# Optimization experiments

Hardware: AMD Instinct MI355X
Metric: run time of the kernel (lower is better)

Reference implementation:

```python
import jax, jax.numpy as jnp
import numpy as np
from jax import lax

EPS_BN = 1e-5
EPS_LN = 1e-5


def setup_inputs() -> dict:
    key = jax.random.key(0)
    ks = jax.random.split(key, 10)
    B, Cin, H, W = 32, 512, 56, 56
    Cout, Cr = 128, 128 // 16  # CBAM reduction 16
    x = jax.random.normal(ks[0], (B, Cin, H, W), dtype=jnp.float32)
    w_proj = jax.random.normal(ks[1], (Cout, Cin), dtype=jnp.float32) * 0.02
    bn_g = jnp.ones((Cout,), jnp.float32)
    bn_b = jnp.zeros((Cout,), jnp.float32)
    bn_m = jax.random.normal(ks[2], (Cout,), dtype=jnp.float32) * 0.1
    bn_v = jax.random.uniform(ks[3], (Cout,), dtype=jnp.float32, minval=0.5, maxval=1.5)
    ca_w1 = jax.random.normal(ks[4], (Cr, Cout), dtype=jnp.float32) * 0.05
    ca_w2 = jax.random.normal(ks[5], (Cout, Cr), dtype=jnp.float32) * 0.05
    sa_w = jax.random.normal(ks[6], (1, 2, 7, 7), dtype=jnp.float32) * 0.05
    ln_g = jnp.ones((Cout,), jnp.float32)
    ln_b = jnp.zeros((Cout,), jnp.float32)
    return dict(x=x, w_proj=w_proj, bn_g=bn_g, bn_b=bn_b, bn_m=bn_m, bn_v=bn_v,
                ca_w1=ca_w1, ca_w2=ca_w2, sa_w=sa_w, ln_g=ln_g, ln_b=ln_b)


def _cbam(x, ca_w1, ca_w2, sa_w):
    # Channel attention: shared MLP on GAP and GMP over spatial dims
    avg = x.mean(axis=(2, 3))  # [B, C]
    mx = x.max(axis=(2, 3))    # [B, C]
    mlp = lambda p: jnp.einsum('cr,br->bc', ca_w2, jax.nn.relu(jnp.einsum('rc,bc->br', ca_w1, p)))
    ca = jax.nn.sigmoid(mlp(avg) + mlp(mx))  # [B, C]
    x = x * ca[:, :, None, None]
    # Spatial attention: channel-wise avg/max -> 7x7 conv -> sigmoid
    s = jnp.stack([x.mean(axis=1), x.max(axis=1)], axis=1)  # [B, 2, H, W]
    sa = lax.conv_general_dilated(s, sa_w, (1, 1), [(3, 3), (3, 3)],
                                  dimension_numbers=('NCHW', 'OIHW', 'NCHW'))
    return x * jax.nn.sigmoid(sa)


def reference(x, w_proj, bn_g, bn_b, bn_m, bn_v, ca_w1, ca_w2, sa_w, ln_g, ln_b):
    # 1x1 conv (no bias) as GEMM over channels
    h = jnp.einsum('bchw,oc->bohw', x, w_proj)
    # BatchNorm (inference) + SiLU
    scale = (bn_g / jnp.sqrt(bn_v + EPS_BN))[None, :, None, None]
    shift = (bn_b - bn_m * bn_g / jnp.sqrt(bn_v + EPS_BN))[None, :, None, None]
    h = h * scale + shift
    h = h * jax.nn.sigmoid(h)  # SiLU
    # CBAM with residual
    y = _cbam(h, ca_w1, ca_w2, sa_w) + h
    # GAP over spatial -> LayerNorm over channels
    y = y.mean(axis=(2, 3))  # [B, C]
    mu = y.mean(axis=-1, keepdims=True)
    var = ((y - mu) ** 2).mean(axis=-1, keepdims=True)
    return (y - mu) / jnp.sqrt(var + EPS_LN) * ln_g + ln_b
```

## Files before the change

kernel.cpp:

```cpp
#include <hip/hip_runtime.h>
#include <hip/hip_bf16.h>

typedef __bf16 bf16x8 __attribute__((ext_vector_type(8)));
typedef float f32x4 __attribute__((ext_vector_type(4)));

#define NB 32
#define CIN 512
#define COUT 128
#define NP 3136
#define WIMG 56

__device__ __forceinline__ unsigned fenc(float f) {
    unsigned u = __float_as_uint(f);
    return (u & 0x80000000u) ? ~u : (u | 0x80000000u);
}
__device__ __forceinline__ float fdec(unsigned e) {
    unsigned u = (e & 0x80000000u) ? (e ^ 0x80000000u) : ~e;
    return __uint_as_float(u);
}
__device__ __forceinline__ float bflo(unsigned u) { return __uint_as_float(u << 16); }
__device__ __forceinline__ float bfhi(unsigned u) { return __uint_as_float(u & 0xffff0000u); }

__device__ __forceinline__ void lds_barrier() {
    asm volatile("s_waitcnt lgkmcnt(0)" ::: "memory");
    __builtin_amdgcn_s_barrier();
    __builtin_amdgcn_sched_barrier(0);
}

__global__ __launch_bounds__(256) void k_wcvt(const float* __restrict__ wp,
                                              ushort* __restrict__ wb,
                                              unsigned* __restrict__ zero8k)
{
    int i = blockIdx.x * 256 + threadIdx.x;
    if (i < 2 * NB * COUT) zero8k[i] = 0u;
    float4 f = *(const float4*)(wp + i * 4);
    ushort4 u;
    __bf16 b0 = (__bf16)f.x, b1 = (__bf16)f.y, b2 = (__bf16)f.z, b3 = (__bf16)f.w;
    u.x = *(ushort*)&b0; u.y = *(ushort*)&b1; u.z = *(ushort*)&b2; u.w = *(ushort*)&b3;
    *(ushort4*)(wb + i * 4) = u;
}

__global__ __launch_bounds__(512, 6) void k_main(
    const float* __restrict__ x, const ushort* __restrict__ wb,
    const float* __restrict__ bn_g, const float* __restrict__ bn_b,
    const float* __restrict__ bn_m, const float* __restrict__ bn_v,
    ushort* __restrict__ hout, float* __restrict__ sumh, unsigned* __restrict__ mxenc)
{
    __shared__ __align__(16) ushort Xs[2][64 * 64];
    __shared__ __align__(16) ushort Ws[2][128 * 64];
    __shared__ float bnss[256];

    const int bid  = blockIdx.x;
    const int swz  = (bid & 7) * 196 + (bid >> 3);
    const int t    = threadIdx.x;
    const int b    = swz / 49;
    const int p0   = (swz % 49) * 64;
    const int lane = t & 63;
    const int l15  = lane & 15;
    const int lg   = lane >> 4;
    const int w    = t >> 6;

    if (t < COUT) {
        float sc = bn_g[t] * rsqrtf(bn_v[t] + 1e-5f);
        bnss[t]        = sc;
        bnss[t + COUT] = bn_b[t] - bn_m[t] * sc;
    }

    const int pr = t & 63;
    const int kg = t >> 6;
    const float* xb = x + ((size_t)b * CIN) * NP + p0 + pr;
    const int xbyte = pr * 128 + ((kg * 16) ^ ((pr & 7) << 4));

    const int ow = t >> 2, kq = t & 3;
    const ushort* wsrc = wb + ow * CIN + kq * 16;
    const int wbyte0 = ow * 128 + ((kq * 32) ^ ((ow & 7) << 4));
    const int wbyte1 = ow * 128 + ((kq * 32 + 16) ^ ((ow & 7) << 4));

    f32x4 acc[4];
#pragma unroll
    for (int nf = 0; nf < 4; ++nf) acc[nf] = (f32x4){0.f, 0.f, 0.f, 0.f};

    float ldx[2][8];
    uint4 ldw0, ldw1;

#pragma unroll
    for (int j = 0; j < 8; ++j) {
        ldx[0][j] = xb[(kg * 8 + j) * NP];
        ldx[1][j] = xb[(64 + kg * 8 + j) * NP];
    }
    ldw0 = *(const uint4*)(wsrc);
    ldw1 = *(const uint4*)(wsrc + 8);
    {
        bf16x8 v8;
#pragma unroll
        for (int j = 0; j < 8; ++j) v8[j] = (__bf16)ldx[0][j];
        *(bf16x8*)((char*)Xs[0] + xbyte) = v8;
        *(uint4*)((char*)Ws[0] + wbyte0) = ldw0;
        *(uint4*)((char*)Ws[0] + wbyte1) = ldw1;
    }

#pragma unroll
    for (int kc = 0; kc < 8; ++kc) {
        lds_barrier();
        if (kc < 6) {
#pragma unroll
            for (int j = 0; j < 8; ++j)
                ldx[kc & 1][j] = xb[((kc + 2) * 64 + kg * 8 + j) * NP];
        }
        if (kc < 7) {
            ldw0 = *(const uint4*)(wsrc + (kc + 1) * 64);
            ldw1 = *(const uint4*)(wsrc + (kc + 1) * 64 + 8);
        }
#pragma unroll
        for (int ks = 0; ks < 2; ++ks) {
            int o = w * 16 + l15;
            bf16x8 af = *(const bf16x8*)((const char*)Ws[kc & 1]
                         + o * 128 + ((ks * 64 + lg * 16) ^ ((o & 7) << 4)));
#pragma unroll
            for (int nf = 0; nf < 4; ++nf) {
                int p = nf * 16 + l15;
                bf16x8 bfr = *(const bf16x8*)((const char*)Xs[kc & 1]
                              + p * 128 + ((ks * 64 + lg * 16) ^ ((p & 7) << 4)));
                acc[nf] = __builtin_amdgcn_mfma_f32_16x16x32_bf16(
                    af, bfr, acc[nf], 0, 0, 0);
            }
        }
        if (kc < 7) {
            bf16x8 v8;
#pragma unroll
            for (int j = 0; j < 8; ++j) v8[j] = (__bf16)ldx[(kc + 1) & 1][j];
            *(bf16x8*)((char*)Xs[(kc + 1) & 1] + xbyte) = v8;
            *(uint4*)((char*)Ws[(kc + 1) & 1] + wbyte0) = ldw0;
            *(uint4*)((char*)Ws[(kc + 1) & 1] + wbyte1) = ldw1;
        }
    }

    __syncthreads();
    ushort* Hs = (ushort*)Xs;
#pragma unroll
    for (int reg = 0; reg < 4; ++reg) {
        int o = w * 16 + lg * 4 + reg;
        float sc = bnss[o], sh = bnss[o + COUT];
        float s_ = 0.f, m_ = -1e30f;
#pragma unroll
        for (int nf = 0; nf < 4; ++nf) {
            float d    = acc[nf][reg];
            float hval = d * sc + sh;
            hval       = hval / (1.f + __expf(-hval));
            s_ += hval;
            m_ = fmaxf(m_, hval);
            __bf16 hb = (__bf16)hval;
            Hs[o * 64 + nf * 16 + l15] = *(ushort*)&hb;
        }
#pragma unroll
        for (int d = 1; d < 16; d <<= 1) {
            s_ += __shfl_xor(s_, d, 64);
            m_ = fmaxf(m_, __shfl_xor(m_, d, 64));
        }
        if (l15 == 0) {
            atomicAdd(&sumh[b * COUT + o], s_);
            atomicMax(&mxenc[b * COUT + o], fenc(m_));
        }
    }
    __syncthreads();
#pragma unroll
    for (int r = 0; r < 2; ++r) {
        int flat = r * 512 + t;
        int orow = flat >> 3, c = flat & 7;
        uint4 v = *(const uint4*)&Hs[orow * 64 + c * 8];
        *(uint4*)&hout[((size_t)b * COUT + orow) * NP + p0 + c * 8] = v;
    }
}

__global__ __launch_bounds__(256) void k_sstat(const ushort* __restrict__ h,
                                               const float* __restrict__ sumh,
                                               const unsigned* __restrict__ mxenc,
                                               const float* __restrict__ w1,
                                               const float* __restrict__ w2,
                                               float* __restrict__ ca,
                                               float* __restrict__ sbuf)
{
    int b = blockIdx.y, z = blockIdx.z;
    int t = threadIdx.x;
    __shared__ float avg[128], mx[128], r1[16], cas[32];
    if (t < 128) {
        avg[t] = sumh[b * COUT + t] * (1.f / (float)NP);
        mx[t]  = fdec(mxenc[b * COUT + t]);
    }
    __syncthreads();
    if (t < 16) {
        int r = t & 7;
        const float* p = (t < 8) ? avg : mx;
        float s = 0.f;
        for (int c = 0; c < 128; ++c) s += w1[r * 128 + c] * p[c];
        r1[t] = fmaxf(s, 0.f);
    }
    __syncthreads();
    if (t < 32) {
        int o = z * 32 + t;
        float s = 0.f;
#pragma unroll
        for (int r = 0; r < 8; ++r) s += w2[o * 8 + r] * (r1[r] + r1[r + 8]);
        float cv = 1.f / (1.f + __expf(-s));
        cas[t] = cv;
        if (blockIdx.x == 0) ca[b * COUT + o] = cv;
    }
    __syncthreads();

    int pp = blockIdx.x * 256 + t;
    if (pp >= NP / 2) return;
    int p = pp * 2;
    const ushort* hb = h + ((size_t)b * COUT + z * 32) * NP + p;
    float s0 = 0.f, s1 = 0.f, m0 = -1e30f, m1 = -1e30f;
#pragma unroll 4
    for (int c = 0; c < 32; ++c) {
        unsigned u = *(const unsigned*)(hb + (size_t)c * NP);
        float cv = cas[c];
        float v0 = bflo(u) * cv;
        float v1 = bfhi(u) * cv;
        s0 += v0; s1 += v1;
        m0 = fmaxf(m0, v0); m1 = fmaxf(m1, v1);
    }
    float* sb = sbuf + ((size_t)(z * NB + b) * 2) * NP;
    sb[p] = s0; sb[p + 1] = s1;
    sb[NP + p] = m0; sb[NP + p + 1] = m1;
}

__global__ __launch_bounds__(256) void k_conv(const float* __restrict__ sbuf,
                                              const float* __restrict__ saw,
                                              float* __restrict__ sigsa)
{
    int band = blockIdx.x, b = blockIdx.y;
    int y0 = band * 7;
    int t = threadIdx.x;
    __shared__ float s[2][13 * WIMG];
    __shared__ float w[98];
    if (t < 98) w[t] = saw[t];
    for (int i = t; i < 13 * WIMG; i += 256) {
        int yy = y0 - 3 + i / WIMG;
        float vs = 0.f, vm = 0.f;
        if (yy >= 0 && yy < WIMG) {
            int p = yy * WIMG + (i % WIMG);
            float ssum = 0.f, smax = -1e30f;
#pragma unroll
            for (int z = 0; z < 4; ++z) {
                const float* sb = sbuf + ((size_t)(z * NB + b) * 2) * NP;
                ssum += sb[p];
                smax = fmaxf(smax, sb[NP + p]);
            }
            vs = ssum * (1.f / (float)COUT);
            vm = smax;
        }
        s[0][i] = vs;
        s[1][i] = vm;
    }
    __syncthreads();
    for (int i = t; i < 7 * WIMG; i += 256) {
        int ly = i / WIMG, px = i % WIMG;
        float a = 0.f;
#pragma unroll
        for (int ch = 0; ch < 2; ++ch) {
#pragma unroll
            for (int dy = 0; dy < 7; ++dy) {
                int li = (ly + dy) * WIMG;
                for (int dx = 0; dx < 7; ++dx) {
                    int xx = px + dx - 3;
                    if (xx < 0 || xx >= WIMG) continue;
                    a += s[ch][li + xx] * w[ch * 49 + dy * 7 + dx];
                }
            }
        }
        sigsa[b * NP + (y0 + ly) * WIMG + px] = 1.f / (1.f + __expf(-a));
    }
}

__global__ __launch_bounds__(256) void k_wsum(const ushort* __restrict__ h,
                                              const float* __restrict__ sigsa,
                                              const float* __restrict__ sumh,
                                              const float* __restrict__ ca,
                                              float* __restrict__ y)
{
    int bo = blockIdx.x;
    int b = bo >> 7;
    int t = threadIdx.x;
    const ushort* hr = h + (size_t)bo * NP;
    const float* sg  = sigsa + (size_t)b * NP;
    float s = 0.f;
#pragma unroll
    for (int i = 0; i < 3; ++i) {
        int q = (i * 256 + t) * 4;
        uint2 u = *(const uint2*)(hr + q);
        float4 g = *(const float4*)(sg + q);
        s += bflo(u.x) * g.x + bfhi(u.x) * g.y + bflo(u.y) * g.z + bfhi(u.y) * g.w;
    }
    if (t < 16) {
        int q = (768 + t) * 4;
        uint2 u = *(const uint2*)(hr + q);
        float4 g = *(const float4*)(sg + q);
        s += bflo(u.x) * g.x + bfhi(u.x) * g.y + bflo(u.y) * g.z + bfhi(u.y) * g.w;
    }
#pragma unroll
    for (int d = 1; d < 64; d <<= 1) s += __shfl_xor(s, d, 64);
    __shared__ float part[4];
    if ((t & 63) == 0) part[t >> 6] = s;
    __syncthreads();
    if (t == 0) {
        float tt = part[0] + part[1] + part[2] + part[3];
        y[bo] = (sumh[bo] + ca[bo] * tt) * (1.f / (float)NP);
    }
}

__global__ void k_ln(const float* __restrict__ y, const float* __restrict__ g,
                     const float* __restrict__ bta, float* __restrict__ out)
{
    int b = blockIdx.x, t = threadIdx.x;
    __shared__ float pr[2], pr2[2];
    float v = y[b * COUT + t];
    float s = v;
#pragma unroll
    for (int d = 1; d < 64; d <<= 1) s += __shfl_xor(s, d, 64);
    if ((t & 63) == 0) pr[t >> 6] = s;
    __syncthreads();
    float mu = (pr[0] + pr[1]) * (1.f / (float)COUT);
    float dv = v - mu;
    float q = dv * dv;
#pragma unroll
    for (int d = 1; d < 64; d <<= 1) q += __shfl_xor(q, d, 64);
    if ((t & 63) == 0) pr2[t >> 6] = q;
    __syncthreads();
    float var = (pr2[0] + pr2[1]) * (1.f / (float)COUT);
    out[b * COUT + t] = dv * rsqrtf(var + 1e-5f) * g[t] + bta[t];
}

extern "C" void kernel_launch(void* const* d_in, const int* in_sizes, int n_in,
                              void* d_out, int out_size, void* d_ws, size_t ws_size,
                              hipStream_t stream)
{
    const float* x     = (const float*)d_in[0];
    const float* wp    = (const float*)d_in[1];
    const float* bn_g  = (const float*)d_in[2];
    const float* bn_b  = (const float*)d_in[3];
    const float* bn_m  = (const float*)d_in[4];
    const float* bn_v  = (const float*)d_in[5];
    const float* ca_w1 = (const float*)d_in[6];
    const float* ca_w2 = (const float*)d_in[7];
    const float* sa_w  = (const float*)d_in[8];
    const float* ln_g  = (const float*)d_in[9];
    const float* ln_b  = (const float*)d_in[10];
    float* out = (float*)d_out;

    char* ws = (char*)d_ws;
    size_t off = 0;
    ushort*   hbuf  = (ushort*)(ws + off);   off += (size_t)NB * COUT * NP * 2;
    float*    sumh  = (float*)(ws + off);    off += NB * COUT * 4;
    unsigned* mxenc = (unsigned*)(ws + off); off += NB * COUT * 4;
    float*    ca    = (float*)(ws + off);    off += NB * COUT * 4;
    float*    sbuf  = (float*)(ws + off);    off += (size_t)4 * NB * 2 * NP * 4;
    float*    sigsa = (float*)(ws + off);    off += (size_t)NB * NP * 4;
    float*    ybuf  = (float*)(ws + off);    off += NB * COUT * 4;
    ushort*   wb16  = (ushort*)(ws + off);   off += (size_t)COUT * CIN * 2;

    k_wcvt<<<64, 256, 0, stream>>>(wp, wb16, (unsigned*)sumh);
    k_main<<<NB * 49, 512, 0, stream>>>(x, wb16, bn_g, bn_b, bn_m, bn_v, hbuf, sumh, mxenc);
    k_sstat<<<dim3(7, NB, 4), 256, 0, stream>>>(hbuf, sumh, mxenc, ca_w1, ca_w2, ca, sbuf);
    k_conv<<<dim3(8, NB), 256, 0, stream>>>(sbuf, sa_w, sigsa);
    k_wsum<<<NB * COUT, 256, 0, stream>>>(hbuf, sigsa, sumh, ca, ybuf);
    k_ln<<<NB, 128, 0, stream>>>(ybuf, ln_g, ln_b, out);
}
```

Measured before the change: 80.85 us.

## Store intermediate activations as FP8 and retile MFMA warps 2x2

The intermediate h tensor is stored as FP8 (e4m3) instead of bf16, halving the bytes written by the GEMM kernel and read by the spatial-stat and weighted-sum kernels. Consumers decode it through a 256-entry shared-memory lookup table. The GEMM warp tiling changes from 16 rows by 64 columns per warp to a 2x2 fragment layout, which reuses A and B fragments across more MFMAs. Per-block channel sum and max are now combined in shared memory before a single set of atomics. FP8 storage lowers the precision of h, which may hurt accuracy against the reference.

```diff
diff --git a/kernel.cpp b/kernel.cpp
--- a/kernel.cpp
+++ b/kernel.cpp
@@ -20,6 +20,23 @@
 }
 __device__ __forceinline__ float bflo(unsigned u) { return __uint_as_float(u << 16); }
 __device__ __forceinline__ float bfhi(unsigned u) { return __uint_as_float(u & 0xffff0000u); }
+
+__device__ __forceinline__ unsigned cvt2_fp8(float a, float b) {
+    unsigned r;
+    asm volatile("v_cvt_pk_fp8_f32 %0, %1, %2" : "=&v"(r) : "v"(a), "v"(b));
+    return r & 0xffffu;
+}
+__device__ __forceinline__ unsigned pack4_fp8(unsigned u01, unsigned u23) {
+    unsigned lo = cvt2_fp8(bflo(u01), bfhi(u01));
+    unsigned hi = cvt2_fp8(bflo(u23), bfhi(u23));
+    return lo | (hi << 16);
+}
+__device__ __forceinline__ float fp8_entry(int v) {
+    unsigned s = (v >> 7) & 1, e = (v >> 3) & 15, m = v & 7;
+    if (e) return __uint_as_float((s << 31) | ((e + 120) << 23) | (m << 20));
+    float f = (float)m * 0x1p-9f;
+    return s ? -f : f;
+}
 
 __device__ __forceinline__ void lds_barrier() {
     asm volatile("s_waitcnt lgkmcnt(0)" ::: "memory");
@@ -44,11 +61,13 @@
     const float* __restrict__ x, const ushort* __restrict__ wb,
     const float* __restrict__ bn_g, const float* __restrict__ bn_b,
     const float* __restrict__ bn_m, const float* __restrict__ bn_v,
-    ushort* __restrict__ hout, float* __restrict__ sumh, unsigned* __restrict__ mxenc)
+    uchar* __restrict__ hout, float* __restrict__ sumh, unsigned* __restrict__ mxenc)
 {
     __shared__ __align__(16) ushort Xs[2][64 * 64];
     __shared__ __align__(16) ushort Ws[2][128 * 64];
     __shared__ float bnss[256];
+    __shared__ float redS[2][COUT];
+    __shared__ float redM[2][COUT];
 
     const int bid  = blockIdx.x;
     const int swz  = (bid & 7) * 196 + (bid >> 3);
@@ -59,6 +78,8 @@
     const int l15  = lane & 15;
     const int lg   = lane >> 4;
     const int w    = t >> 6;
+    const int wm   = w >> 1;
+    const int wn   = w & 1;
 
     if (t < COUT) {
         float sc = bn_g[t] * rsqrtf(bn_v[t] + 1e-5f);
@@ -76,9 +97,11 @@
     const int wbyte0 = ow * 128 + ((kq * 32) ^ ((ow & 7) << 4));
     const int wbyte1 = ow * 128 + ((kq * 32 + 16) ^ ((ow & 7) << 4));
 
-    f32x4 acc[4];
-#pragma unroll
-    for (int nf = 0; nf < 4; ++nf) acc[nf] = (f32x4){0.f, 0.f, 0.f, 0.f};
+    f32x4 acc[2][2];
+#pragma unroll
+    for (int mf = 0; mf < 2; ++mf)
+#pragma unroll
+        for (int nf = 0; nf < 2; ++nf) acc[mf][nf] = (f32x4){0.f, 0.f, 0.f, 0.f};
 
     float ldx[2][8];
     uint4 ldw0, ldw1;
@@ -113,17 +136,25 @@
         }
 #pragma unroll
         for (int ks = 0; ks < 2; ++ks) {
-            int o = w * 16 + l15;
-            bf16x8 af = *(const bf16x8*)((const char*)Ws[kc & 1]
-                         + o * 128 + ((ks * 64 + lg * 16) ^ ((o & 7) << 4)));
-#pragma unroll
-            for (int nf = 0; nf < 4; ++nf) {
-                int p = nf * 16 + l15;
-                bf16x8 bfr = *(const bf16x8*)((const char*)Xs[kc & 1]
-                              + p * 128 + ((ks * 64 + lg * 16) ^ ((p & 7) << 4)));
-                acc[nf] = __builtin_amdgcn_mfma_f32_16x16x32_bf16(
-                    af, bfr, acc[nf], 0, 0, 0);
-            }
+            bf16x8 af[2], bfr[2];
+#pragma unroll
+            for (int mf = 0; mf < 2; ++mf) {
+                int o = wm * 32 + mf * 16 + l15;
+                af[mf] = *(const bf16x8*)((const char*)Ws[kc & 1]
+                          + o * 128 + ((ks * 64 + lg * 16) ^ ((o & 7) << 4)));
+            }
+#pragma unroll
+            for (int nf = 0; nf < 2; ++nf) {
+                int p = wn * 32 + nf * 16 + l15;
+                bfr[nf] = *(const bf16x8*)((const char*)Xs[kc & 1]
+                           + p * 128 + ((ks * 64 + lg * 16) ^ ((p & 7) << 4)));
+            }
+#pragma unroll
+            for (int mf = 0; mf < 2; ++mf)
+#pragma unroll
+                for (int nf = 0; nf < 2; ++nf)
+                    acc[mf][nf] = __builtin_amdgcn_mfma_f32_16x16x32_bf16(
+                        af[mf], bfr[nf], acc[mf][nf], 0, 0, 0);
         }
         if (kc < 7) {
             bf16x8 v8;
@@ -138,41 +169,52 @@
     __syncthreads();
     ushort* Hs = (ushort*)Xs;
 #pragma unroll
-    for (int reg = 0; reg < 4; ++reg) {
-        int o = w * 16 + lg * 4 + reg;
-        float sc = bnss[o], sh = bnss[o + COUT];
-        float s_ = 0.f, m_ = -1e30f;
-#pragma unroll
-        for (int nf = 0; nf < 4; ++nf) {
-            float d    = acc[nf][reg];
-            float hval = d * sc + sh;
-            hval       = hval / (1.f + __expf(-hval));
-            s_ += hval;
-            m_ = fmaxf(m_, hval);
-            __bf16 hb = (__bf16)hval;
-            Hs[o * 64 + nf * 16 + l15] = *(ushort*)&hb;
-        }
-#pragma unroll
-        for (int d = 1; d < 16; d <<= 1) {
-            s_ += __shfl_xor(s_, d, 64);
-            m_ = fmaxf(m_, __shfl_xor(m_, d, 64));
-        }
-        if (l15 == 0) {
-            atomicAdd(&sumh[b * COUT + o], s_);
-            atomicMax(&mxenc[b * COUT + o], fenc(m_));
-        }
-    }
-    __syncthreads();
-#pragma unroll
-    for (int r = 0; r < 2; ++r) {
-        int flat = r * 512 + t;
-        int orow = flat >> 3, c = flat & 7;
-        uint4 v = *(const uint4*)&Hs[orow * 64 + c * 8];
-        *(uint4*)&hout[((size_t)b * COUT + orow) * NP + p0 + c * 8] = v;
-    }
-}
-
-__global__ __launch_bounds__(256) void k_sstat(const ushort* __restrict__ h,
+    for (int mf = 0; mf < 2; ++mf) {
+#pragma unroll
+        for (int reg = 0; reg < 4; ++reg) {
+            int o = wm * 32 + mf * 16 + lg * 4 + reg;
+            float sc = bnss[o], sh = bnss[o + COUT];
+            float s_ = 0.f, m_ = -1e30f;
+#pragma unroll
+            for (int nf = 0; nf < 2; ++nf) {
+                float d    = acc[mf][nf][reg];
+                float hval = d * sc + sh;
+                hval       = hval / (1.f + __expf(-hval));
+                s_ += hval;
+                m_ = fmaxf(m_, hval);
+                __bf16 hb = (__bf16)hval;
+                Hs[o * 64 + wn * 32 + nf * 16 + l15] = *(ushort*)&hb;
+            }
+#pragma unroll
+            for (int d = 1; d < 16; d <<= 1) {
+                s_ += __shfl_xor(s_, d, 64);
+                m_ = fmaxf(m_, __shfl_xor(m_, d, 64));
+            }
+            if (l15 == 0) {
+                redS[wn][o] = s_;
+                redM[wn][o] = m_;
+            }
+        }
+    }
+    __syncthreads();
+    if (t < COUT) {
+        atomicAdd(&sumh[b * COUT + t], redS[0][t] + redS[1][t]);
+        atomicMax(&mxenc[b * COUT + t], fenc(fmaxf(redM[0][t], redM[1][t])));
+    }
+    {
+        int orow = t >> 2, c = t & 3;
+        uint4 a  = *(const uint4*)&Hs[orow * 64 + c * 16];
+        uint4 b4 = *(const uint4*)&Hs[orow * 64 + c * 16 + 8];
+        uint4 o4;
+        o4.x = pack4_fp8(a.x, a.y);
+        o4.y = pack4_fp8(a.z, a.w);
+        o4.z = pack4_fp8(b4.x, b4.y);
+        o4.w = pack4_fp8(b4.z, b4.w);
+        *(uint4*)&hout[((size_t)b * COUT + orow) * NP + p0 + c * 16] = o4;
+    }
+}
+
+__global__ __launch_bounds__(256) void k_sstat(const uchar* __restrict__ h,
                                                const float* __restrict__ sumh,
                                                const unsigned* __restrict__ mxenc,
                                                const float* __restrict__ w1,
@@ -182,7 +224,8 @@
 {
     int b = blockIdx.y, z = blockIdx.z;
     int t = threadIdx.x;
-    __shared__ float avg[128], mx[128], r1[16], cas[32];
+    __shared__ float avg[128], mx[128], r1[16], cas[32], tab[256];
+    tab[t] = fp8_entry(t);
     if (t < 128) {
         avg[t] = sumh[b * COUT + t] * (1.f / (float)NP);
         mx[t]  = fdec(mxenc[b * COUT + t]);
@@ -207,23 +250,27 @@
     }
     __syncthreads();
 
-    int pp = blockIdx.x * 256 + t;
-    if (pp >= NP / 2) return;
-    int p = pp * 2;
-    const ushort* hb = h + ((size_t)b * COUT + z * 32) * NP + p;
-    float s0 = 0.f, s1 = 0.f, m0 = -1e30f, m1 = -1e30f;
+    int idx = blockIdx.x * 256 + t;
+    if (idx >= NP / 4) return;
+    int p = idx * 4;
+    const uchar* hb = h + ((size_t)(b * COUT + z * 32)) * NP + p;
+    float s0 = 0.f, s1 = 0.f, s2 = 0.f, s3 = 0.f;
+    float m0 = -1e30f, m1 = -1e30f, m2 = -1e30f, m3 = -1e30f;
 #pragma unroll 4
     for (int c = 0; c < 32; ++c) {
         unsigned u = *(const unsigned*)(hb + (size_t)c * NP);
         float cv = cas[c];
-        float v0 = bflo(u) * cv;
-        float v1 = bfhi(u) * cv;
-        s0 += v0; s1 += v1;
+        float v0 = tab[u & 255] * cv;
+        float v1 = tab[(u >> 8) & 255] * cv;
+        float v2 = tab[(u >> 16) & 255] * cv;
+        float v3 = tab[u >> 24] * cv;
+        s0 += v0; s1 += v1; s2 += v2; s3 += v3;
         m0 = fmaxf(m0, v0); m1 = fmaxf(m1, v1);
+        m2 = fmaxf(m2, v2); m3 = fmaxf(m3, v3);
     }
     float* sb = sbuf + ((size_t)(z * NB + b) * 2) * NP;
-    sb[p] = s0; sb[p + 1] = s1;
-    sb[NP + p] = m0; sb[NP + p + 1] = m1;
+    *(float4*)&sb[p]      = make_float4(s0, s1, s2, s3);
+    *(float4*)&sb[NP + p] = make_float4(m0, m1, m2, m3);
 }
 
 __global__ __launch_bounds__(256) void k_conv(const float* __restrict__ sbuf,
@@ -274,7 +321,7 @@
     }
 }
 
-__global__ __launch_bounds__(256) void k_wsum(const ushort* __restrict__ h,
+__global__ __launch_bounds__(256) void k_wsum(const uchar* __restrict__ h,
                                               const float* __restrict__ sigsa,
                                               const float* __restrict__ sumh,
                                               const float* __restrict__ ca,
@@ -283,25 +330,30 @@
     int bo = blockIdx.x;
     int b = bo >> 7;
     int t = threadIdx.x;
-    const ushort* hr = h + (size_t)bo * NP;
+    __shared__ float tab[256];
+    __shared__ float part[4];
+    tab[t] = fp8_entry(t);
+    __syncthreads();
+    const uchar* hr = h + (size_t)bo * NP;
     const float* sg  = sigsa + (size_t)b * NP;
     float s = 0.f;
 #pragma unroll
     for (int i = 0; i < 3; ++i) {
-        int q = (i * 256 + t) * 4;
-        uint2 u = *(const uint2*)(hr + q);
-        float4 g = *(const float4*)(sg + q);
-        s += bflo(u.x) * g.x + bfhi(u.x) * g.y + bflo(u.y) * g.z + bfhi(u.y) * g.w;
+        int q = i * 256 + t;
+        unsigned u = *(const unsigned*)(hr + q * 4);
+        float4 g = *(const float4*)(sg + q * 4);
+        s += tab[u & 255] * g.x + tab[(u >> 8) & 255] * g.y
+           + tab[(u >> 16) & 255] * g.z + tab[u >> 24] * g.w;
     }
     if (t < 16) {
-        int q = (768 + t) * 4;
-        uint2 u = *(const uint2*)(hr + q);
-        float4 g = *(const float4*)(sg + q);
-        s += bflo(u.x) * g.x + bfhi(u.x) * g.y + bflo(u.y) * g.z + bfhi(u.y) * g.w;
+        int q = 768 + t;
+        unsigned u = *(const unsigned*)(hr + q * 4);
+        float4 g = *(const float4*)(sg + q * 4);
+        s += tab[u & 255] * g.x + tab[(u >> 8) & 255] * g.y
+           + tab[(u >> 16) & 255] * g.z + tab[u >> 24] * g.w;
     }
 #pragma unroll
     for (int d = 1; d < 64; d <<= 1) s += __shfl_xor(s, d, 64);
-    __shared__ float part[4];
     if ((t & 63) == 0) part[t >> 6] = s;
     __syncthreads();
     if (t == 0) {
@@ -351,7 +403,7 @@
 
     char* ws = (char*)d_ws;
     size_t off = 0;
-    ushort*   hbuf  = (ushort*)(ws + off);   off += (size_t)NB * COUT * NP * 2;
+    uchar*    hbuf  = (uchar*)(ws + off);    off += (size_t)NB * COUT * NP;
     float*    sumh  = (float*)(ws + off);    off += NB * COUT * 4;
     unsigned* mxenc = (unsigned*)(ws + off); off += NB * COUT * 4;
     float*    ca    = (float*)(ws + off);    off += NB * COUT * 4;
@@ -362,7 +414,7 @@
 
     k_wcvt<<<64, 256, 0, stream>>>(wp, wb16, (unsigned*)sumh);
     k_main<<<NB * 49, 512, 0, stream>>>(x, wb16, bn_g, bn_b, bn_m, bn_v, hbuf, sumh, mxenc);
-    k_sstat<<<dim3(7, NB, 4), 256, 0, stream>>>(hbuf, sumh, mxenc, ca_w1, ca_w2, ca, sbuf);
+    k_sstat<<<dim3(4, NB, 4), 256, 0, stream>>>(hbuf, sumh, mxenc, ca_w1, ca_w2, ca, sbuf);
     k_conv<<<dim3(8, NB), 256, 0, stream>>>(sbuf, sa_w, sigsa);
     k_wsum<<<NB * COUT, 256, 0, stream>>>(hbuf, sigsa, sumh, ca, ybuf);
     k_ln<<<NB, 128, 0, stream>>>(ybuf, ln_g, ln_b, out);
```

After: 79.73 us, median of 3. Within noise of the previous version (-1.4%).
